# Optimization experiments

Measured on AMD Instinct MI355X. Metric: run time of the kernel, lower is better.

## Reference

```python
import jax, jax.numpy as jnp
import numpy as np

DIM = 192
HEAD_DIM = 32
HEADS = DIM // HEAD_DIM  # 6
H = W = 56
WS = 7            # window size
SS = 3            # shift size
L = WS * WS       # tokens per window = 49
NH, NW = H // WS, W // WS
NWIN = NH * NW    # windows per image = 64
SCALE = HEAD_DIM ** -0.5


def _rel_indices():
    # matches ShiftedWindowAttention.get_indices
    a = np.arange(WS)
    y1, x1, y2, x2 = np.meshgrid(a, a, a, a, indexing='ij')
    idx = (y1 - y2 + WS - 1) * (2 * WS - 1) + (x1 - x2 + WS - 1)
    return idx.reshape(-1)  # [WS^4] = [L*L]


def _shift_mask():
    # matches ShiftedWindowAttention.generate_mask -> bool [NWIN, L, L]
    region = np.zeros((H, W), dtype=np.int32)
    slices = [slice(0, -WS), slice(-WS, -SS), slice(-SS, None)]
    r = 0
    for i in slices:
        for j in slices:
            region[i, j] = r
            r += 1
    win = region.reshape(NH, WS, NW, WS).transpose(0, 2, 1, 3).reshape(NWIN, L)
    return (win[:, None, :] - win[:, :, None]) != 0


_REL_IDX = _rel_indices()
_MASK = _shift_mask()


def setup_inputs() -> dict:
    key = jax.random.key(0)
    ks = jax.random.split(key, 4)
    B = 32
    return {
        'x': jax.random.normal(ks[0], (B, H * W, DIM), jnp.float32),
        'w_qkv': jax.random.normal(ks[1], (3 * DIM, DIM), jnp.float32) * 0.02,
        'b_qkv': jnp.zeros((3 * DIM,), jnp.float32),
        'w_out': jax.random.normal(ks[2], (DIM, DIM), jnp.float32) * 0.02,
        'b_out': jnp.zeros((DIM,), jnp.float32),
        'pos_enc': jax.random.normal(ks[3], (HEADS, (2 * WS - 1) ** 2), jnp.float32) * 0.02,
    }


def reference(x, w_qkv, b_qkv, w_out, b_out, pos_enc):
    B = x.shape[0]
    # to windows (with cyclic shift)
    xg = x.reshape(B, H, W, DIM)
    xg = jnp.roll(xg, (-SS, -SS), axis=(1, 2))
    xw = xg.reshape(B, NH, WS, NW, WS, DIM).transpose(0, 1, 3, 2, 4, 5)
    xw = xw.reshape(B * NWIN, L, DIM)
    # qkv projection: torch Linear -> x @ W^T + b
    qkv = xw @ w_qkv.T + b_qkv                      # [BW, L, 3*DIM]
    qkv = qkv.reshape(B * NWIN, L, 3, HEADS, HEAD_DIM)
    qkv = qkv.transpose(2, 0, 3, 1, 4)              # [3, BW, heads, L, hd]
    q, k, v = qkv[0], qkv[1], qkv[2]
    # attention scores + gathered relative position bias
    att = jnp.einsum('whid,whjd->whij', q, k) * SCALE  # [BW, heads, L, L]
    rel = pos_enc[:, _REL_IDX].reshape(HEADS, L, L)    # gather per head
    att = att + rel
    # shift mask
    mask = jnp.asarray(_MASK)                          # [NWIN, L, L]
    att = att.reshape(B, NWIN, HEADS, L, L)
    att = jnp.where(mask[None, :, None, :, :], -jnp.inf, att)
    att = att.reshape(B * NWIN, HEADS, L, L)
    att = jax.nn.softmax(att, axis=-1)
    # weighted values, merge heads
    out = jnp.einsum('whij,whjd->whid', att, v)        # [BW, heads, L, hd]
    out = out.transpose(0, 2, 1, 3).reshape(B * NWIN, L, DIM)
    out = out @ w_out.T + b_out
    # from windows (undo shift)
    out = out.reshape(B, NH, NW, WS, WS, DIM).transpose(0, 1, 3, 2, 4, 5)
    out = out.reshape(B, H, W, DIM)
    out = jnp.roll(out, (SS, SS), axis=(1, 2))
    return out.reshape(B, H * W, DIM)
```

## Files before the change

kernel.cpp:

```cpp
#include <hip/hip_runtime.h>
#include <hip/hip_bf16.h>
#include <cstddef>
#include <cstdint>

typedef _Float16 half_t;
typedef _Float16 half8  __attribute__((ext_vector_type(8)));
typedef _Float16 half4v __attribute__((ext_vector_type(4)));
typedef float    f32x4  __attribute__((ext_vector_type(4)));

#define SCALE 0.17677669529663687f


__global__ __launch_bounds__(256) void convert_w(
    const float* __restrict__ w_qkv, const float* __restrict__ w_out,
    half_t* __restrict__ wq, half_t* __restrict__ wo)
{
    int i = blockIdx.x * 256 + threadIdx.x;
    if (i < 110592) {
        int u8 = i >> 3, e = i & 7;
        int c  = u8 & 15;
        int g  = (u8 >> 4) & 3;
        int ks = (u8 >> 6) % 6;
        int ct = u8 / 384;
        wq[i] = (half_t)w_qkv[(16 * ct + c) * 192 + ks * 32 + g * 8 + e];
    } else {
        int j = i - 110592;
        if (j < 36864) {
            int u8 = j >> 3, e = j & 7;
            int c  = u8 & 15;
            int g  = (u8 >> 4) & 3;
            int ks = (u8 >> 6) % 6;
            int q  = u8 / 384;
            wo[j] = (half_t)w_out[(16 * q + c) * 192 + ks * 32 + g * 8 + e];
        }
    }
}

__global__ __launch_bounds__(256) void build_bias(
    const float* __restrict__ pos_enc, half_t* __restrict__ mb)
{
    int idx = blockIdx.x * 256 + threadIdx.x;
    int j   = idx & 63;
    int i   = (idx >> 6) & 63;
    int hmc = idx >> 12;
    int h   = hmc % 6, mc = hmc / 6;
    float v = -60000.f;
    if (i < 49 && j < 49) {
        int yi = i / 7, xi = i - 7 * yi;
        int yj = j / 7, xj = j - 7 * yj;
        int ri = ((mc & 2) ? (yi < 4 ? 1 : 2) : 0) * 3 + ((mc & 1) ? (xi < 4 ? 1 : 2) : 0);
        int rj = ((mc & 2) ? (yj < 4 ? 1 : 2) : 0) * 3 + ((mc & 1) ? (xj < 4 ? 1 : 2) : 0);
        if (ri == rj) v = pos_enc[h * 169 + (yi - yj + 6) * 13 + (xi - xj + 6)];
    }
    mb[idx] = (half_t)v;
}

__global__ __launch_bounds__(512, 4) void swin_qkv(
    const float*  __restrict__ x,
    const half_t* __restrict__ wqfrag,
    const float*  __restrict__ b_qkv,
    half_t* __restrict__ qws,
    half_t* __restrict__ kws,
    half_t* __restrict__ vtws)
{
    __shared__ half_t sW[2304 * 8];

    const int tid  = threadIdx.x;
    const int wave = tid >> 6, lane = tid & 63;
    const int c    = lane & 15, g = lane >> 4;
    const int widx = wave >> 1, mh = wave & 1;
    const int w    = blockIdx.x * 4 + widx;
    const int b    = w >> 6, win = w & 63, nh = win >> 3, nw = win & 7;

    half8 xf[2][6];
    #pragma unroll
    for (int t = 0; t < 2; ++t) {
        int tok = 32 * mh + 16 * t + c;
        if (tok < 49) {
            int ty = tok / 7, tx = tok - ty * 7;
            int sy = nh * 7 + ty + 3; if (sy >= 56) sy -= 56;
            int sx = nw * 7 + tx + 3; if (sx >= 56) sx -= 56;
            const float* xr = x + ((size_t)b * 3136 + sy * 56 + sx) * 192 + g * 8;
            #pragma unroll
            for (int ks = 0; ks < 6; ++ks) {
                float4 v0 = *(const float4*)(xr + ks * 32);
                float4 v1 = *(const float4*)(xr + ks * 32 + 4);
                xf[t][ks] = (half8){(half_t)v0.x, (half_t)v0.y, (half_t)v0.z, (half_t)v0.w,
                                    (half_t)v1.x, (half_t)v1.y, (half_t)v1.z, (half_t)v1.w};
            }
        } else {
            #pragma unroll
            for (int ks = 0; ks < 6; ++ks)
                xf[t][ks] = (half8){(half_t)0.f, (half_t)0.f, (half_t)0.f, (half_t)0.f,
                                    (half_t)0.f, (half_t)0.f, (half_t)0.f, (half_t)0.f};
        }
    }

    #pragma unroll
    for (int ch = 0; ch < 6; ++ch) {
        #pragma unroll
        for (int p = 0; p < 5; ++p) {
            int u = tid + p * 512;
            if (u < 2304) {
                const half_t* src = wqfrag + ((size_t)ch * 2304 + u) * 8;
                half_t* dst = &sW[u * 8];
                __builtin_amdgcn_global_load_lds(
                    (const __attribute__((address_space(1))) unsigned int*)src,
                    (__attribute__((address_space(3))) unsigned int*)dst, 16, 0, 0);
            }
        }
        __syncthreads();

        #pragma unroll
        for (int ctl = 0; ctl < 6; ++ctl) {
            const int ct = ch * 6 + ctl;
            f32x4 a0 = (f32x4){0.f, 0.f, 0.f, 0.f};
            f32x4 a1 = (f32x4){0.f, 0.f, 0.f, 0.f};
            #pragma unroll
            for (int ks = 0; ks < 6; ++ks) {
                half8 bF = *(const half8*)&sW[(ctl * 384 + ks * 64 + g * 16 + c) * 8];
                a0 = __builtin_amdgcn_mfma_f32_16x16x32_f16(xf[0][ks], bF, a0, 0, 0, 0);
                a1 = __builtin_amdgcn_mfma_f32_16x16x32_f16(xf[1][ks], bF, a1, 0, 0, 0);
            }
            const int kind = ct / 12, rem = ct - 12 * kind;
            const int h = rem >> 1, d = ((rem & 1) << 4) + c;
            const float bias = b_qkv[16 * ct + c];
            const int wh = w * 6 + h;
            if (kind == 2) {
                #pragma unroll
                for (int t = 0; t < 2; ++t) {
                    f32x4 a = t ? a1 : a0;
                    int tok0 = 32 * mh + 16 * t + 4 * g;
                    if (tok0 <= 48) {
                        half4v pv = (half4v){(half_t)(a[0] + bias), (half_t)(a[1] + bias),
                                             (half_t)(a[2] + bias), (half_t)(a[3] + bias)};
                        *(half4v*)(vtws + (size_t)(wh * 32 + d) * 52 + tok0) = pv;
                    }
                }
            } else {
                half_t* dstp = (kind == 0) ? qws : kws;
                #pragma unroll
                for (int t = 0; t < 2; ++t) {
                    f32x4 a = t ? a1 : a0;
                    #pragma unroll
                    for (int r = 0; r < 4; ++r) {
                        int tok = 32 * mh + 16 * t + 4 * g + r;
                        if (tok < 49)
                            dstp[((size_t)wh * 49 + tok) * 32 + d] = (half_t)(a[r] + bias);
                    }
                }
            }
        }
        __syncthreads();
    }
}

__global__ __launch_bounds__(512, 4) void swin_attn_proj(
    const half_t* __restrict__ qws,
    const half_t* __restrict__ kws,
    const half_t* __restrict__ vtws,
    const half_t* __restrict__ mb16,
    const half_t* __restrict__ wofrag,
    const float*  __restrict__ b_out,
    float* __restrict__ out)
{
    __shared__ __align__(16) half_t sK[1536 * 8];
    __shared__ __align__(16) half_t sAf[6 * 4 * 64 * 8];

    const int w    = blockIdx.x;
    const int b    = w >> 6, win = w & 63, nh = win >> 3, nw = win & 7;
    const int tid  = threadIdx.x;
    const int wave = tid >> 6, lane = tid & 63;
    const int c    = lane & 15, g = lane >> 4;
    const int ti   = wave & 3, hf = wave >> 2;
    const int i_tok = 16 * ti + c;
    const int mc   = 2 * (nh == 7) + (nw == 7);

    {
        const half_t* src = kws + (size_t)w * 9408;
        #pragma unroll
        for (int rnd = 0; rnd < 3; ++rnd) {
            int u = tid + rnd * 512;
            __builtin_amdgcn_global_load_lds(
                (const __attribute__((address_space(1))) unsigned int*)(src + u * 8),
                (__attribute__((address_space(3))) unsigned int*)(&sK[u * 8]), 16, 0, 0);
        }
    }

    half8  qA, qB;
    half4v bA[4], bB[4];
    half4v vA[8], vB[8];

#define LOADH(QF, BF, VF, hh) do {                                              \
        const int wh_ = w * 6 + (hh);                                           \
        QF = *(const half8*)(qws + ((size_t)wh_ * 49 + i_tok) * 32 + g * 8);    \
        const half_t* mrow_ = mb16 + ((size_t)(mc * 6 + (hh)) * 64 + i_tok) * 64; \
        _Pragma("unroll")                                                       \
        for (int tj_ = 0; tj_ < 4; ++tj_)                                       \
            BF[tj_] = *(const half4v*)(mrow_ + 16 * tj_ + 4 * g);               \
        const half_t* vh_ = vtws + (size_t)wh_ * 1664;                          \
        _Pragma("unroll")                                                       \
        for (int tj_ = 0; tj_ < 4; ++tj_) {                                     \
            VF[2 * tj_]     = *(const half4v*)(vh_ + c * 52 + 16 * tj_ + 4 * g);        \
            VF[2 * tj_ + 1] = *(const half4v*)(vh_ + (16 + c) * 52 + 16 * tj_ + 4 * g); \
        }                                                                       \
    } while (0)

    LOADH(qA, bA, vA, 3 * hf);
    __syncthreads();

    #pragma unroll
    for (int p = 0; p < 3; ++p) {
        const int h = 3 * hf + p;
        if (p == 0) LOADH(qB, bB, vB, h + 1);
        if (p == 1) LOADH(qA, bA, vA, h + 1);

        const half8&  qf = (p == 1) ? qB : qA;
        const half4v* bf = (p == 1) ? bB : bA;
        const half4v* vf = (p == 1) ? vB : vA;

        half8 kf[4];
        #pragma unroll
        for (int tj = 0; tj < 4; ++tj)
            kf[tj] = *(const half8*)&sK[((size_t)h * 49 + 16 * tj + c) * 32 + g * 8];

        f32x4 st[4];
        #pragma unroll
        for (int tj = 0; tj < 4; ++tj) {
            f32x4 z = (f32x4){0.f, 0.f, 0.f, 0.f};
            st[tj] = __builtin_amdgcn_mfma_f32_16x16x32_f16(kf[tj], qf, z, 0, 0, 0);
        }
        #pragma unroll
        for (int tj = 0; tj < 4; ++tj)
            #pragma unroll
            for (int r = 0; r < 4; ++r)
                st[tj][r] = st[tj][r] * SCALE + (float)bf[tj][r];

        float m = st[0][0];
        #pragma unroll
        for (int tj = 0; tj < 4; ++tj)
            #pragma unroll
            for (int r = 0; r < 4; ++r) m = fmaxf(m, st[tj][r]);
        m = fmaxf(m, __shfl_xor(m, 16));
        m = fmaxf(m, __shfl_xor(m, 32));
        float sum = 0.f;
        #pragma unroll
        for (int tj = 0; tj < 4; ++tj)
            #pragma unroll
            for (int r = 0; r < 4; ++r) {
                float e = __expf(st[tj][r] - m);
                st[tj][r] = e;
                sum += e;
            }
        sum += __shfl_xor(sum, 16);
        sum += __shfl_xor(sum, 32);
        float inv = 1.0f / sum;
        half4v pa[4];
        #pragma unroll
        for (int tj = 0; tj < 4; ++tj)
            pa[tj] = (half4v){(half_t)(st[tj][0] * inv), (half_t)(st[tj][1] * inv),
                              (half_t)(st[tj][2] * inv), (half_t)(st[tj][3] * inv)};

        f32x4 o0 = (f32x4){0.f, 0.f, 0.f, 0.f};
        f32x4 o1 = (f32x4){0.f, 0.f, 0.f, 0.f};
        #pragma unroll
        for (int tj = 0; tj < 4; ++tj) {
            o0 = __builtin_amdgcn_mfma_f32_16x16x16f16(vf[2 * tj],     pa[tj], o0, 0, 0, 0);
            o1 = __builtin_amdgcn_mfma_f32_16x16x16f16(vf[2 * tj + 1], pa[tj], o1, 0, 0, 0);
        }
        {
            int base = (((h * 4 + ti) * 64 + (g >> 1) * 16 + c) << 3) + (g & 1) * 4;
            *(half4v*)&sAf[base] =
                (half4v){(half_t)o0[0], (half_t)o0[1], (half_t)o0[2], (half_t)o0[3]};
            *(half4v*)&sAf[base + 256] =
                (half4v){(half_t)o1[0], (half_t)o1[1], (half_t)o1[2], (half_t)o1[3]};
        }
    }
#undef LOADH
    __syncthreads();

    {
        f32x4 pacc[6];
        float bo[6];
        #pragma unroll
        for (int q = 0; q < 6; ++q) {
            pacc[q] = (f32x4){0.f, 0.f, 0.f, 0.f};
            bo[q] = b_out[16 * (6 * hf + q) + c];
        }
        #pragma unroll
        for (int ks = 0; ks < 6; ++ks) {
            half8 aF = *(const half8*)&sAf[((ks * 4 + ti) * 64 + lane) * 8];
            #pragma unroll
            for (int q = 0; q < 6; ++q) {
                int ct = 6 * hf + q;
                half8 bF = *(const half8*)(wofrag + ((size_t)(ct * 6 + ks) * 64 + lane) * 8);
                pacc[q] = __builtin_amdgcn_mfma_f32_16x16x32_f16(aF, bF, pacc[q], 0, 0, 0);
            }
        }
        #pragma unroll
        for (int r = 0; r < 4; ++r) {
            int tok = 16 * ti + g * 4 + r;
            if (tok < 49) {
                int ty = tok / 7, tx = tok - ty * 7;
                int dy = nh * 7 + ty + 3; if (dy >= 56) dy -= 56;
                int dx = nw * 7 + tx + 3; if (dx >= 56) dx -= 56;
                float* op = out + ((size_t)b * 3136 + dy * 56 + dx) * 192;
                #pragma unroll
                for (int q = 0; q < 6; ++q)
                    op[16 * (6 * hf + q) + c] = pacc[q][r] + bo[q];
            }
        }
    }
}

extern "C" void kernel_launch(void* const* d_in, const int* in_sizes, int n_in,
                              void* d_out, int out_size, void* d_ws, size_t ws_size,
                              hipStream_t stream) {
    const float* x       = (const float*)d_in[0];
    const float* w_qkv   = (const float*)d_in[1];
    const float* b_qkv   = (const float*)d_in[2];
    const float* w_out   = (const float*)d_in[3];
    const float* b_out   = (const float*)d_in[4];
    const float* pos_enc = (const float*)d_in[5];
    float* out = (float*)d_out;

    half_t* wqf  = (half_t*)d_ws;
    half_t* mb16 = (half_t*)d_ws;
    half_t* wof  = (half_t*)((char*)d_ws + 221184);
    half_t* qws  = (half_t*)((char*)d_ws + 294912);
    half_t* kws  = (half_t*)((char*)d_ws + 38830080);
    half_t* vtws = (half_t*)((char*)d_ws + 77365248);

    convert_w<<<dim3(576), dim3(256), 0, stream>>>(w_qkv, w_out, wqf, wof);
    swin_qkv<<<dim3(512), dim3(512), 0, stream>>>(x, wqf, b_qkv, qws, kws, vtws);
    build_bias<<<dim3(384), dim3(256), 0, stream>>>(pos_enc, mb16);
    swin_attn_proj<<<dim3(2048), dim3(512), 0, stream>>>(
        qws, kws, vtws, mb16, wof, b_out, out);
}
```

Measured before the change: 130.7 us.

## Split QKV work across four waves per window and pad V-transpose stride

```diff
diff --git a/kernel.cpp b/kernel.cpp
--- a/kernel.cpp
+++ b/kernel.cpp
@@ -61,21 +61,21 @@
     const float*  __restrict__ b_qkv,
     half_t* __restrict__ qws,
     half_t* __restrict__ kws,
-    half_t* __restrict__ vtws)
+    half_t* __restrict__ vtws,
+    int vts)
 {
     __shared__ half_t sW[2304 * 8];
 
     const int tid  = threadIdx.x;
     const int wave = tid >> 6, lane = tid & 63;
     const int c    = lane & 15, g = lane >> 4;
-    const int widx = wave >> 1, mh = wave & 1;
-    const int w    = blockIdx.x * 4 + widx;
+    const int widx = wave >> 2, mt = wave & 3;
+    const int w    = blockIdx.x * 2 + widx;
     const int b    = w >> 6, win = w & 63, nh = win >> 3, nw = win & 7;
 
-    half8 xf[2][6];
-    #pragma unroll
-    for (int t = 0; t < 2; ++t) {
-        int tok = 32 * mh + 16 * t + c;
+    half8 xf[6];
+    {
+        int tok = 16 * mt + c;
         if (tok < 49) {
             int ty = tok / 7, tx = tok - ty * 7;
             int sy = nh * 7 + ty + 3; if (sy >= 56) sy -= 56;
@@ -85,14 +85,14 @@
             for (int ks = 0; ks < 6; ++ks) {
                 float4 v0 = *(const float4*)(xr + ks * 32);
                 float4 v1 = *(const float4*)(xr + ks * 32 + 4);
-                xf[t][ks] = (half8){(half_t)v0.x, (half_t)v0.y, (half_t)v0.z, (half_t)v0.w,
-                                    (half_t)v1.x, (half_t)v1.y, (half_t)v1.z, (half_t)v1.w};
+                xf[ks] = (half8){(half_t)v0.x, (half_t)v0.y, (half_t)v0.z, (half_t)v0.w,
+                                 (half_t)v1.x, (half_t)v1.y, (half_t)v1.z, (half_t)v1.w};
             }
         } else {
             #pragma unroll
             for (int ks = 0; ks < 6; ++ks)
-                xf[t][ks] = (half8){(half_t)0.f, (half_t)0.f, (half_t)0.f, (half_t)0.f,
-                                    (half_t)0.f, (half_t)0.f, (half_t)0.f, (half_t)0.f};
+                xf[ks] = (half8){(half_t)0.f, (half_t)0.f, (half_t)0.f, (half_t)0.f,
+                                 (half_t)0.f, (half_t)0.f, (half_t)0.f, (half_t)0.f};
         }
     }
 
@@ -115,39 +115,29 @@
         for (int ctl = 0; ctl < 6; ++ctl) {
             const int ct = ch * 6 + ctl;
             f32x4 a0 = (f32x4){0.f, 0.f, 0.f, 0.f};
-            f32x4 a1 = (f32x4){0.f, 0.f, 0.f, 0.f};
             #pragma unroll
             for (int ks = 0; ks < 6; ++ks) {
                 half8 bF = *(const half8*)&sW[(ctl * 384 + ks * 64 + g * 16 + c) * 8];
-                a0 = __builtin_amdgcn_mfma_f32_16x16x32_f16(xf[0][ks], bF, a0, 0, 0, 0);
-                a1 = __builtin_amdgcn_mfma_f32_16x16x32_f16(xf[1][ks], bF, a1, 0, 0, 0);
+                a0 = __builtin_amdgcn_mfma_f32_16x16x32_f16(xf[ks], bF, a0, 0, 0, 0);
             }
             const int kind = ct / 12, rem = ct - 12 * kind;
             const int h = rem >> 1, d = ((rem & 1) << 4) + c;
             const float bias = b_qkv[16 * ct + c];
             const int wh = w * 6 + h;
             if (kind == 2) {
-                #pragma unroll
-                for (int t = 0; t < 2; ++t) {
-                    f32x4 a = t ? a1 : a0;
-                    int tok0 = 32 * mh + 16 * t + 4 * g;
-                    if (tok0 <= 48) {
-                        half4v pv = (half4v){(half_t)(a[0] + bias), (half_t)(a[1] + bias),
-                                             (half_t)(a[2] + bias), (half_t)(a[3] + bias)};
-                        *(half4v*)(vtws + (size_t)(wh * 32 + d) * 52 + tok0) = pv;
-                    }
+                int tok0 = 16 * mt + 4 * g;
+                if (tok0 <= 48) {
+                    half4v pv = (half4v){(half_t)(a0[0] + bias), (half_t)(a0[1] + bias),
+                                         (half_t)(a0[2] + bias), (half_t)(a0[3] + bias)};
+                    *(half4v*)(vtws + (size_t)(wh * 32 + d) * vts + tok0) = pv;
                 }
             } else {
                 half_t* dstp = (kind == 0) ? qws : kws;
                 #pragma unroll
-                for (int t = 0; t < 2; ++t) {
-                    f32x4 a = t ? a1 : a0;
-                    #pragma unroll
-                    for (int r = 0; r < 4; ++r) {
-                        int tok = 32 * mh + 16 * t + 4 * g + r;
-                        if (tok < 49)
-                            dstp[((size_t)wh * 49 + tok) * 32 + d] = (half_t)(a[r] + bias);
-                    }
+                for (int r = 0; r < 4; ++r) {
+                    int tok = 16 * mt + 4 * g + r;
+                    if (tok < 49)
+                        dstp[((size_t)wh * 49 + tok) * 32 + d] = (half_t)(a0[r] + bias);
                 }
             }
         }
@@ -162,7 +152,8 @@
     const half_t* __restrict__ mb16,
     const half_t* __restrict__ wofrag,
     const float*  __restrict__ b_out,
-    float* __restrict__ out)
+    float* __restrict__ out,
+    int vts)
 {
     __shared__ __align__(16) half_t sK[1536 * 8];
     __shared__ __align__(16) half_t sAf[6 * 4 * 64 * 8];
@@ -198,11 +189,11 @@
         _Pragma("unroll")                                                       \
         for (int tj_ = 0; tj_ < 4; ++tj_)                                       \
             BF[tj_] = *(const half4v*)(mrow_ + 16 * tj_ + 4 * g);               \
-        const half_t* vh_ = vtws + (size_t)wh_ * 1664;                          \
+        const half_t* vh_ = vtws + (size_t)wh_ * 32 * vts;                      \
         _Pragma("unroll")                                                       \
         for (int tj_ = 0; tj_ < 4; ++tj_) {                                     \
-            VF[2 * tj_]     = *(const half4v*)(vh_ + c * 52 + 16 * tj_ + 4 * g);        \
-            VF[2 * tj_ + 1] = *(const half4v*)(vh_ + (16 + c) * 52 + 16 * tj_ + 4 * g); \
+            VF[2 * tj_]     = *(const half4v*)(vh_ + c * vts + 16 * tj_ + 4 * g);        \
+            VF[2 * tj_ + 1] = *(const half4v*)(vh_ + (16 + c) * vts + 16 * tj_ + 4 * g); \
         }                                                                       \
     } while (0)
 
@@ -331,9 +322,12 @@
     half_t* kws  = (half_t*)((char*)d_ws + 38830080);
     half_t* vtws = (half_t*)((char*)d_ws + 77365248);
 
+    const size_t need64 = 77365248ULL + 2048ULL * 6 * 32 * 64 * 2;
+    const int vts = (ws_size >= need64) ? 64 : 52;
+
     convert_w<<<dim3(576), dim3(256), 0, stream>>>(w_qkv, w_out, wqf, wof);
-    swin_qkv<<<dim3(512), dim3(512), 0, stream>>>(x, wqf, b_qkv, qws, kws, vtws);
+    swin_qkv<<<dim3(1024), dim3(512), 0, stream>>>(x, wqf, b_qkv, qws, kws, vtws, vts);
     build_bias<<<dim3(384), dim3(256), 0, stream>>>(pos_enc, mb16);
     swin_attn_proj<<<dim3(2048), dim3(512), 0, stream>>>(
-        qws, kws, vtws, mb16, wof, b_out, out);
-}
+        qws, kws, vtws, mb16, wof, b_out, out, vts);
+}
```

Result: slower. 173.7 us (+32.9%).

## Drop LDS weight staging in QKV kernel and use one window per block

Applied to the files above, without the earlier changes.

```diff
diff --git a/kernel.cpp b/kernel.cpp
--- a/kernel.cpp
+++ b/kernel.cpp
@@ -55,7 +55,7 @@
     mb[idx] = (half_t)v;
 }
 
-__global__ __launch_bounds__(512, 4) void swin_qkv(
+__global__ __launch_bounds__(128, 4) void swin_qkv(
     const float*  __restrict__ x,
     const half_t* __restrict__ wqfrag,
     const float*  __restrict__ b_qkv,
@@ -63,14 +63,12 @@
     half_t* __restrict__ kws,
     half_t* __restrict__ vtws)
 {
-    __shared__ half_t sW[2304 * 8];
-
     const int tid  = threadIdx.x;
-    const int wave = tid >> 6, lane = tid & 63;
+    const int mh   = tid >> 6, lane = tid & 63;
     const int c    = lane & 15, g = lane >> 4;
-    const int widx = wave >> 1, mh = wave & 1;
-    const int w    = blockIdx.x * 4 + widx;
+    const int w    = blockIdx.x;
     const int b    = w >> 6, win = w & 63, nh = win >> 3, nw = win & 7;
+    const int wh0  = w * 6;
 
     half8 xf[2][6];
     #pragma unroll
@@ -96,63 +94,56 @@
         }
     }
 
-    #pragma unroll
-    for (int ch = 0; ch < 6; ++ch) {
-        #pragma unroll
-        for (int p = 0; p < 5; ++p) {
-            int u = tid + p * 512;
-            if (u < 2304) {
-                const half_t* src = wqfrag + ((size_t)ch * 2304 + u) * 8;
-                half_t* dst = &sW[u * 8];
-                __builtin_amdgcn_global_load_lds(
-                    (const __attribute__((address_space(1))) unsigned int*)src,
-                    (__attribute__((address_space(3))) unsigned int*)dst, 16, 0, 0);
-            }
-        }
-        __syncthreads();
-
-        #pragma unroll
-        for (int ctl = 0; ctl < 6; ++ctl) {
-            const int ct = ch * 6 + ctl;
-            f32x4 a0 = (f32x4){0.f, 0.f, 0.f, 0.f};
-            f32x4 a1 = (f32x4){0.f, 0.f, 0.f, 0.f};
-            #pragma unroll
-            for (int ks = 0; ks < 6; ++ks) {
-                half8 bF = *(const half8*)&sW[(ctl * 384 + ks * 64 + g * 16 + c) * 8];
-                a0 = __builtin_amdgcn_mfma_f32_16x16x32_f16(xf[0][ks], bF, a0, 0, 0, 0);
-                a1 = __builtin_amdgcn_mfma_f32_16x16x32_f16(xf[1][ks], bF, a1, 0, 0, 0);
-            }
-            const int kind = ct / 12, rem = ct - 12 * kind;
-            const int h = rem >> 1, d = ((rem & 1) << 4) + c;
-            const float bias = b_qkv[16 * ct + c];
-            const int wh = w * 6 + h;
-            if (kind == 2) {
-                #pragma unroll
-                for (int t = 0; t < 2; ++t) {
-                    f32x4 a = t ? a1 : a0;
-                    int tok0 = 32 * mh + 16 * t + 4 * g;
-                    if (tok0 <= 48) {
-                        half4v pv = (half4v){(half_t)(a[0] + bias), (half_t)(a[1] + bias),
-                                             (half_t)(a[2] + bias), (half_t)(a[3] + bias)};
-                        *(half4v*)(vtws + (size_t)(wh * 32 + d) * 52 + tok0) = pv;
-                    }
-                }
-            } else {
-                half_t* dstp = (kind == 0) ? qws : kws;
-                #pragma unroll
-                for (int t = 0; t < 2; ++t) {
-                    f32x4 a = t ? a1 : a0;
-                    #pragma unroll
-                    for (int r = 0; r < 4; ++r) {
-                        int tok = 32 * mh + 16 * t + 4 * g + r;
-                        if (tok < 49)
-                            dstp[((size_t)wh * 49 + tok) * 32 + d] = (half_t)(a[r] + bias);
-                    }
-                }
-            }
-        }
-        __syncthreads();
-    }
+#define DO_CT(CT, KIND) do {                                                      \
+        const int ct_ = (CT);                                                     \
+        const half_t* wp_ = wqfrag + ((size_t)ct_ * 384 + lane) * 8;              \
+        half8 bf_[6];                                                             \
+        _Pragma("unroll")                                                         \
+        for (int ks = 0; ks < 6; ++ks) bf_[ks] = *(const half8*)(wp_ + ks * 512); \
+        f32x4 a0_ = (f32x4){0.f, 0.f, 0.f, 0.f};                                  \
+        f32x4 a1_ = (f32x4){0.f, 0.f, 0.f, 0.f};                                  \
+        _Pragma("unroll")                                                         \
+        for (int ks = 0; ks < 6; ++ks) {                                          \
+            a0_ = __builtin_amdgcn_mfma_f32_16x16x32_f16(xf[0][ks], bf_[ks], a0_, 0, 0, 0); \
+            a1_ = __builtin_amdgcn_mfma_f32_16x16x32_f16(xf[1][ks], bf_[ks], a1_, 0, 0, 0); \
+        }                                                                         \
+        const int rem_ = ct_ - 12 * (KIND);                                       \
+        const int h_ = rem_ >> 1, d_ = ((rem_ & 1) << 4) + c;                     \
+        const float bias_ = b_qkv[16 * ct_ + c];                                  \
+        const int wh_ = wh0 + h_;                                                 \
+        if ((KIND) == 2) {                                                        \
+            _Pragma("unroll")                                                     \
+            for (int t = 0; t < 2; ++t) {                                         \
+                f32x4 a_ = t ? a1_ : a0_;                                         \
+                int tok0_ = 32 * mh + 16 * t + 4 * g;                             \
+                if (tok0_ <= 48) {                                                \
+                    half4v pv_ = (half4v){(half_t)(a_[0] + bias_), (half_t)(a_[1] + bias_), \
+                                          (half_t)(a_[2] + bias_), (half_t)(a_[3] + bias_)}; \
+                    *(half4v*)(vtws + (size_t)(wh_ * 32 + d_) * 52 + tok0_) = pv_; \
+                }                                                                 \
+            }                                                                     \
+        } else {                                                                  \
+            half_t* dstp_ = ((KIND) == 0) ? qws : kws;                            \
+            _Pragma("unroll")                                                     \
+            for (int t = 0; t < 2; ++t) {                                         \
+                f32x4 a_ = t ? a1_ : a0_;                                         \
+                _Pragma("unroll")                                                 \
+                for (int r = 0; r < 4; ++r) {                                     \
+                    int tok_ = 32 * mh + 16 * t + 4 * g + r;                      \
+                    if (tok_ < 49)                                                \
+                        dstp_[((size_t)wh_ * 49 + tok_) * 32 + d_] = (half_t)(a_[r] + bias_); \
+                }                                                                 \
+            }                                                                     \
+        }                                                                         \
+    } while (0)
+
+    #pragma unroll 4
+    for (int ct = 0; ct < 12; ++ct) DO_CT(ct, 0);
+    #pragma unroll 4
+    for (int ct = 12; ct < 24; ++ct) DO_CT(ct, 1);
+    #pragma unroll 4
+    for (int ct = 24; ct < 36; ++ct) DO_CT(ct, 2);
+#undef DO_CT
 }
 
 __global__ __launch_bounds__(512, 4) void swin_attn_proj(
@@ -332,7 +323,7 @@
     half_t* vtws = (half_t*)((char*)d_ws + 77365248);
 
     convert_w<<<dim3(576), dim3(256), 0, stream>>>(w_qkv, w_out, wqf, wof);
-    swin_qkv<<<dim3(512), dim3(512), 0, stream>>>(x, wqf, b_qkv, qws, kws, vtws);
+    swin_qkv<<<dim3(2048), dim3(128), 0, stream>>>(x, wqf, b_qkv, qws, kws, vtws);
     build_bias<<<dim3(384), dim3(256), 0, stream>>>(pos_enc, mb16);
     swin_attn_proj<<<dim3(2048), dim3(512), 0, stream>>>(
         qws, kws, vtws, mb16, wof, b_out, out);
```

After: 135.7 us. 3.8% more time.

## Split QKV projection per window and q/k/v kind, load weights directly

Applied to the files above, without the earlier changes.

```diff
diff --git a/kernel.cpp b/kernel.cpp
--- a/kernel.cpp
+++ b/kernel.cpp
@@ -55,7 +55,7 @@
     mb[idx] = (half_t)v;
 }
 
-__global__ __launch_bounds__(512, 4) void swin_qkv(
+__global__ __launch_bounds__(128, 8) void swin_qkv(
     const float*  __restrict__ x,
     const half_t* __restrict__ wqfrag,
     const float*  __restrict__ b_qkv,
@@ -63,14 +63,13 @@
     half_t* __restrict__ kws,
     half_t* __restrict__ vtws)
 {
-    __shared__ half_t sW[2304 * 8];
-
     const int tid  = threadIdx.x;
-    const int wave = tid >> 6, lane = tid & 63;
+    const int mh   = tid >> 6, lane = tid & 63;
     const int c    = lane & 15, g = lane >> 4;
-    const int widx = wave >> 1, mh = wave & 1;
-    const int w    = blockIdx.x * 4 + widx;
+    const int w    = blockIdx.x;
+    const int kind = blockIdx.y;
     const int b    = w >> 6, win = w & 63, nh = win >> 3, nw = win & 7;
+    const int wh0  = w * 6;
 
     half8 xf[2][6];
     #pragma unroll
@@ -96,62 +95,48 @@
         }
     }
 
-    #pragma unroll
-    for (int ch = 0; ch < 6; ++ch) {
-        #pragma unroll
-        for (int p = 0; p < 5; ++p) {
-            int u = tid + p * 512;
-            if (u < 2304) {
-                const half_t* src = wqfrag + ((size_t)ch * 2304 + u) * 8;
-                half_t* dst = &sW[u * 8];
-                __builtin_amdgcn_global_load_lds(
-                    (const __attribute__((address_space(1))) unsigned int*)src,
-                    (__attribute__((address_space(3))) unsigned int*)dst, 16, 0, 0);
-            }
-        }
-        __syncthreads();
-
-        #pragma unroll
-        for (int ctl = 0; ctl < 6; ++ctl) {
-            const int ct = ch * 6 + ctl;
-            f32x4 a0 = (f32x4){0.f, 0.f, 0.f, 0.f};
-            f32x4 a1 = (f32x4){0.f, 0.f, 0.f, 0.f};
-            #pragma unroll
-            for (int ks = 0; ks < 6; ++ks) {
-                half8 bF = *(const half8*)&sW[(ctl * 384 + ks * 64 + g * 16 + c) * 8];
-                a0 = __builtin_amdgcn_mfma_f32_16x16x32_f16(xf[0][ks], bF, a0, 0, 0, 0);
-                a1 = __builtin_amdgcn_mfma_f32_16x16x32_f16(xf[1][ks], bF, a1, 0, 0, 0);
-            }
-            const int kind = ct / 12, rem = ct - 12 * kind;
-            const int h = rem >> 1, d = ((rem & 1) << 4) + c;
-            const float bias = b_qkv[16 * ct + c];
-            const int wh = w * 6 + h;
-            if (kind == 2) {
+    half_t* const qk_dst = (kind == 0) ? qws : kws;
+
+    #pragma unroll 4
+    for (int q12 = 0; q12 < 12; ++q12) {
+        const int ct  = kind * 12 + q12;
+        const half_t* wp = wqfrag + ((size_t)ct * 384 + lane) * 8;
+        half8 bf[6];
+        #pragma unroll
+        for (int ks = 0; ks < 6; ++ks) bf[ks] = *(const half8*)(wp + ks * 512);
+        f32x4 a0 = (f32x4){0.f, 0.f, 0.f, 0.f};
+        f32x4 a1 = (f32x4){0.f, 0.f, 0.f, 0.f};
+        #pragma unroll
+        for (int ks = 0; ks < 6; ++ks) {
+            a0 = __builtin_amdgcn_mfma_f32_16x16x32_f16(xf[0][ks], bf[ks], a0, 0, 0, 0);
+            a1 = __builtin_amdgcn_mfma_f32_16x16x32_f16(xf[1][ks], bf[ks], a1, 0, 0, 0);
+        }
+        const int h = q12 >> 1, d = ((q12 & 1) << 4) + c;
+        const float bias = b_qkv[16 * ct + c];
+        const int wh = wh0 + h;
+        if (kind == 2) {
+            #pragma unroll
+            for (int t = 0; t < 2; ++t) {
+                f32x4 a = t ? a1 : a0;
+                int tok0 = 32 * mh + 16 * t + 4 * g;
+                if (tok0 <= 48) {
+                    half4v pv = (half4v){(half_t)(a[0] + bias), (half_t)(a[1] + bias),
+                                         (half_t)(a[2] + bias), (half_t)(a[3] + bias)};
+                    *(half4v*)(vtws + (size_t)(wh * 32 + d) * 52 + tok0) = pv;
+                }
+            }
+        } else {
+            #pragma unroll
+            for (int t = 0; t < 2; ++t) {
+                f32x4 a = t ? a1 : a0;
                 #pragma unroll
-                for (int t = 0; t < 2; ++t) {
-                    f32x4 a = t ? a1 : a0;
-                    int tok0 = 32 * mh + 16 * t + 4 * g;
-                    if (tok0 <= 48) {
-                        half4v pv = (half4v){(half_t)(a[0] + bias), (half_t)(a[1] + bias),
-                                             (half_t)(a[2] + bias), (half_t)(a[3] + bias)};
-                        *(half4v*)(vtws + (size_t)(wh * 32 + d) * 52 + tok0) = pv;
-                    }
+                for (int r = 0; r < 4; ++r) {
+                    int tok = 32 * mh + 16 * t + 4 * g + r;
+                    if (tok < 49)
+                        qk_dst[((size_t)wh * 49 + tok) * 32 + d] = (half_t)(a[r] + bias);
                 }
-            } else {
-                half_t* dstp = (kind == 0) ? qws : kws;
-                #pragma unroll
-                for (int t = 0; t < 2; ++t) {
-                    f32x4 a = t ? a1 : a0;
-                    #pragma unroll
-                    for (int r = 0; r < 4; ++r) {
-                        int tok = 32 * mh + 16 * t + 4 * g + r;
-                        if (tok < 49)
-                            dstp[((size_t)wh * 49 + tok) * 32 + d] = (half_t)(a[r] + bias);
-                    }
-                }
-            }
-        }
-        __syncthreads();
+            }
+        }
     }
 }
 
@@ -332,7 +317,7 @@
     half_t* vtws = (half_t*)((char*)d_ws + 77365248);
 
     convert_w<<<dim3(576), dim3(256), 0, stream>>>(w_qkv, w_out, wqf, wof);
-    swin_qkv<<<dim3(512), dim3(512), 0, stream>>>(x, wqf, b_qkv, qws, kws, vtws);
+    swin_qkv<<<dim3(2048, 3), dim3(128), 0, stream>>>(x, wqf, b_qkv, qws, kws, vtws);
     build_bias<<<dim3(384), dim3(256), 0, stream>>>(pos_enc, mb16);
     swin_attn_proj<<<dim3(2048), dim3(512), 0, stream>>>(
         qws, kws, vtws, mb16, wof, b_out, out);
```

Measured after the change: 279.2 us. 114% more time.
